# Kernel optimization log

Measured on AMD Instinct MI355X. Metric: run time of the kernel, lower is better.

The kernel has to match this reference:

```python
import jax, jax.numpy as jnp
import numpy as np

B, C, H, W = 2, 128, 96, 96
HEADS, WIN, M = 4, 7, 16
HD = C // HEADS
N = H * W
K = WIN * WIN


def _unfold(xp, h, w, win):
    wins = jnp.stack([xp[:, :, i:i + h, j:j + w]
                      for i in range(win) for j in range(win)], axis=-1)  # [B,C_,h,w,K]
    b, c = xp.shape[0], xp.shape[1]
    return wins.reshape(b, c, h * w, win * win).transpose(0, 2, 3, 1)


def setup_inputs() -> dict:
    key = jax.random.key(0)
    ks = jax.random.split(key, 12)
    s = 0.02
    return {
        "x": jax.random.normal(ks[0], (B, C, H, W), dtype=jnp.float32),
        "phi": jax.random.normal(ks[1], (B, M, H, W), dtype=jnp.float32),
        "Wq": jax.random.normal(ks[2], (C, C), dtype=jnp.float32) * s,
        "bq": jax.random.normal(ks[3], (C,), dtype=jnp.float32) * s,
        "Wk": jax.random.normal(ks[4], (C, C), dtype=jnp.float32) * s,
        "bk": jax.random.normal(ks[5], (C,), dtype=jnp.float32) * s,
        "Wv": jax.random.normal(ks[6], (C, C), dtype=jnp.float32) * s,
        "bv": jax.random.normal(ks[7], (C,), dtype=jnp.float32) * s,
        "Wo": jax.random.normal(ks[8], (C, C), dtype=jnp.float32) * s,
        "bo": jax.random.normal(ks[9], (C,), dtype=jnp.float32) * s,
        "log_alpha": jnp.zeros((), dtype=jnp.float32),  # alpha = 1.0
        "beta": jnp.full((HEADS,), 0.5, dtype=jnp.float32),
    }


def reference(x, phi, Wq, bq, Wk, bk, Wv, bv, Wo, bo, log_alpha, beta):
    pad = WIN // 2
    scale = HD ** -0.5
    normalizer = np.sqrt(2.0 * M).astype(np.float32)

    x_pad = jnp.pad(x, ((0, 0), (0, 0), (pad, pad), (pad, pad)))
    phi_pad = jnp.pad(phi, ((0, 0), (0, 0), (pad, pad), (pad, pad)), constant_values=1.0)

    x_flat = x.reshape(B, C, N).transpose(0, 2, 1)          # [B,N,C]
    q = (x_flat @ Wq + bq).reshape(B, N, HEADS, HD)

    xu = _unfold(x_pad, H, W, WIN)                          # [B,N,K,C]
    k = (xu @ Wk + bk).reshape(B, N, K, HEADS, HD)
    v = (xu @ Wv + bv).reshape(B, N, K, HEADS, HD)

    logits = jnp.einsum('bnhd,bnkhd->bhnk', q, k) * scale   # [B,HEADS,N,K]

    phi_u = _unfold(phi_pad, H, W, WIN)                     # [B,N,K,M]
    phi_c = phi.reshape(B, M, N).transpose(0, 2, 1)[:, :, None, :]  # [B,N,1,M]
    diff_sq = ((phi_c - phi_u) ** 2).sum(-1)                # [B,N,K]
    log_k_geo = -jnp.exp(log_alpha) * diff_sq / normalizer
    logits = logits + beta[None, :, None, None] * log_k_geo[:, None]

    attn = jax.nn.softmax(logits, axis=-1)                  # [B,HEADS,N,K]
    out = jnp.einsum('bhnk,bnkhd->bnhd', attn, v).reshape(B, N, C)
    out = (out @ Wo + bo).transpose(0, 2, 1).reshape(B, C, H, W)
    return out
```

## Files before the change

kernel.cpp:

```cpp
#include <hip/hip_runtime.h>

typedef unsigned int uint;
typedef __attribute__((ext_vector_type(8))) short bf16x8;
typedef __attribute__((ext_vector_type(4))) float f32x4;

#define B_ 2
#define C_ 128
#define H_ 96
#define W_ 96
#define HEADS_ 4
#define HD_ 32
#define M_ 16
#define WIN_ 7
#define PAD_ 3
#define N_ (H_*W_)
#define HP_ (H_+2*PAD_)
#define HP2_ (HP_*HP_)
#define KW_ (WIN_*WIN_)
#define TILE_ 8
#define HALO_ (TILE_+WIN_-1)
#define NHALO_ (HALO_*HALO_)

static __device__ __forceinline__ uint f2bf(float f) {
    uint u = __float_as_uint(f);
    u = (u + 0x7fffu + ((u >> 16) & 1u)) >> 16;
    return u & 0xffffu;
}
static __device__ __forceinline__ uint pack2(float a, float b) {
    return f2bf(a) | (f2bf(b) << 16);
}
static __device__ __forceinline__ float bf_lo(uint u){ return __uint_as_float(u << 16); }
static __device__ __forceinline__ float bf_hi(uint u){ return __uint_as_float(u & 0xffff0000u); }

static __device__ __forceinline__ float dot2bf(uint a, uint b, float c) {
    float d;
    asm("v_dot2_f32_bf16 %0, %1, %2, %3" : "=v"(d) : "v"(a), "v"(b), "v"(c));
    return d;
}

template<int CTRL>
static __device__ __forceinline__ float dpp_mov(float v) {
    return __int_as_float(__builtin_amdgcn_update_dpp(
        0, __float_as_int(v), CTRL, 0xF, 0xF, false));
}
#define DPP_XOR1(v)  dpp_mov<0xB1>(v)
#define DPP_XOR2(v)  dpp_mov<0x4E>(v)
#define DPP_BCAST0(v) dpp_mov<0x00>(v)
#define DPP_BCAST1(v) dpp_mov<0x55>(v)
#define DPP_BCAST2(v) dpp_mov<0xAA>(v)
#define DPP_BCAST3(v) dpp_mov<0xFF>(v)

#define SWZ(row, c2) ((c2) ^ (((row) & 7) << 2))


__global__ __launch_bounds__(256) void pad_fill(
    const float* __restrict__ phi, const float* __restrict__ bk, const float* __restrict__ bv,
    uint* __restrict__ KVp, float* __restrict__ PhiT)
{
    int idx = blockIdx.x * 256 + threadIdx.x;
    if (idx >= B_*HP2_) return;
    int b  = idx / HP2_;
    int pp = idx % HP2_;
    int py = pp / HP_, px = pp % HP_;
    bool interior = (py >= PAD_ && py < H_+PAD_ && px >= PAD_ && px < W_+PAD_);
    if (!interior) {
        #pragma unroll
        for (int h = 0; h < HEADS_; ++h) {
            size_t base = ((size_t)(b*HEADS_+h)*HP2_ + pp) * 32;
            #pragma unroll
            for (int q4i = 0; q4i < 4; ++q4i) {
                const float* kb8 = bk + h*HD_ + q4i*8;
                const float* vb8 = bv + h*HD_ + q4i*8;
                uint4 ku, vu;
                ku.x = pack2(kb8[0],kb8[1]); ku.y = pack2(kb8[2],kb8[3]);
                ku.z = pack2(kb8[4],kb8[5]); ku.w = pack2(kb8[6],kb8[7]);
                vu.x = pack2(vb8[0],vb8[1]); vu.y = pack2(vb8[2],vb8[3]);
                vu.z = pack2(vb8[4],vb8[5]); vu.w = pack2(vb8[6],vb8[7]);
                ((uint4*)(KVp + base))[q4i]     = ku;
                ((uint4*)(KVp + base))[4 + q4i] = vu;
            }
        }
    }
    size_t pb = ((size_t)b*HP2_ + pp) * M_;
    if (interior) {
        int y = py - PAD_, xx = px - PAD_;
        #pragma unroll
        for (int m = 0; m < M_; ++m)
            PhiT[pb + m] = phi[((size_t)b*M_ + m)*N_ + y*W_ + xx];
    } else {
        #pragma unroll
        for (int m = 0; m < M_; ++m) PhiT[pb + m] = 1.0f;
    }
}

__global__ __launch_bounds__(256, 3) void qkv_proj(
    const float* __restrict__ x,
    const float* __restrict__ Wq, const float* __restrict__ bq,
    const float* __restrict__ Wk, const float* __restrict__ bk,
    const float* __restrict__ Wv, const float* __restrict__ bv,
    float* __restrict__ Qp, uint* __restrict__ KVp)
{
    __shared__ uint ldsA[128*64];
    __shared__ uint ldsB[64*64];

    const int t  = threadIdx.x;
    const int n0 = blockIdx.x * 64;
    const int b  = blockIdx.y;
    const int pj = blockIdx.z;
    const float* Wsrc = (pj == 0) ? Wq : (pj == 1) ? Wk : Wv;
    const float* bsrc = (pj == 0) ? bq : (pj == 1) ? bk : bv;

    for (int idx = t; idx < 128*64; idx += 256) {
        int co = idx & 127, c2 = idx >> 7;
        float w0 = Wsrc[(size_t)(2*c2  )*C_ + co];
        float w1 = Wsrc[(size_t)(2*c2+1)*C_ + co];
        ldsA[co*64 + SWZ(co, c2)] = pack2(w0, w1);
    }
    const float* xb = x + (size_t)b*C_*N_;
    for (int idx = t; idx < 64*64; idx += 256) {
        int pix = idx & 63, c2 = idx >> 6;
        float a0 = xb[(size_t)(2*c2  )*N_ + n0 + pix];
        float a1 = xb[(size_t)(2*c2+1)*N_ + n0 + pix];
        ldsB[pix*64 + SWZ(pix, c2)] = pack2(a0, a1);
    }
    __syncthreads();

    const int lane = t & 63, w = t >> 6;
    const int q = lane >> 4, r16 = lane & 15;
    const int sw = (r16 & 7) << 2;

    f32x4 acc[2][4];
    #pragma unroll
    for (int cf = 0; cf < 2; ++cf) {
        float4 b4 = *(const float4*)(bsrc + (2*w+cf)*16 + q*4);
        f32x4 bi = {b4.x, b4.y, b4.z, b4.w};
        #pragma unroll
        for (int pf = 0; pf < 4; ++pf) acc[cf][pf] = bi;
    }

    #pragma unroll
    for (int kk = 0; kk < 4; ++kk) {
        int kbase = kk*16 + q*4;
        bf16x8 af[2], bfr[4];
        #pragma unroll
        for (int cf = 0; cf < 2; ++cf) {
            int row = (2*w+cf)*16 + r16;
            af[cf] = *(const bf16x8*)&ldsA[row*64 + (kbase ^ sw)];
        }
        #pragma unroll
        for (int pf = 0; pf < 4; ++pf) {
            int row = pf*16 + r16;
            bfr[pf] = *(const bf16x8*)&ldsB[row*64 + (kbase ^ sw)];
        }
        #pragma unroll
        for (int cf = 0; cf < 2; ++cf)
            #pragma unroll
            for (int pf = 0; pf < 4; ++pf)
                acc[cf][pf] = __builtin_amdgcn_mfma_f32_16x16x32_bf16(
                    af[cf], bfr[pf], acc[cf][pf], 0, 0, 0);
    }

    if (pj == 0) {
        #pragma unroll
        for (int pf = 0; pf < 4; ++pf) {
            int n = n0 + pf*16 + r16;
            #pragma unroll
            for (int cf = 0; cf < 2; ++cf) {
                int co0 = (2*w+cf)*16 + q*4;
                *(f32x4*)(Qp + ((size_t)b*N_ + n)*C_ + co0) = acc[cf][pf];
            }
        }
    } else {
        int rowb[4];
        #pragma unroll
        for (int pf = 0; pf < 4; ++pf) {
            int n = n0 + pf*16 + r16;
            int y = n / W_, xx = n - y*W_;
            rowb[pf] = (y+PAD_)*HP_ + xx + PAD_;
        }
        const int ubase = (pj == 1) ? 0 : 16;
        #pragma unroll
        for (int cf = 0; cf < 2; ++cf) {
            int co0 = (2*w+cf)*16 + q*4;
            int h   = co0 >> 5;
            int u   = ubase + ((co0 & 31) >> 1);
            uint* kvb = KVp + (size_t)(b*HEADS_+h)*HP2_*32;
            #pragma unroll
            for (int pf = 0; pf < 4; ++pf) {
                uint2 uu;
                uu.x = pack2(acc[cf][pf][0], acc[cf][pf][1]);
                uu.y = pack2(acc[cf][pf][2], acc[cf][pf][3]);
                *(uint2*)(kvb + (size_t)rowb[pf]*32 + u) = uu;
            }
        }
    }
}

__global__ __launch_bounds__(256, 3) void attn(
    const float* __restrict__ Qp, const uint* __restrict__ KVp,
    const float* __restrict__ PhiT, const float* __restrict__ log_alpha,
    const float* __restrict__ beta, float* __restrict__ AO)
{
    __shared__ uint4  kl[NHALO_*4];
    __shared__ uint4  vl[NHALO_*4];
    __shared__ float4 pl[NHALO_*4];

    const int t  = threadIdx.x;
    const int h  = blockIdx.y;
    const int b  = blockIdx.z;
    const int bx = blockIdx.x;
    const int tile = ((bx & 7) * 18) + (bx >> 3);
    const int y0 = (tile / (W_/TILE_)) * TILE_;
    const int x0 = (tile % (W_/TILE_)) * TILE_;

    const uint* kvb = KVp + (size_t)(b*HEADS_+h)*HP2_*32;
    for (int idx = t; idx < NHALO_*8; idx += 256) {
        int hp = idx >> 3, u4 = idx & 7;
        int hy = hp / HALO_, hx = hp % HALO_;
        size_t rowb = (size_t)(y0+hy)*HP_ + (x0+hx);
        uint4 val = *(const uint4*)(kvb + rowb*32 + u4*4);
        if (u4 < 4) kl[hp*4 + u4] = val;
        else        vl[hp*4 + (u4-4)] = val;
    }
    const float* pbase = PhiT + (size_t)b*HP2_*M_;
    for (int idx = t; idx < NHALO_*4; idx += 256) {
        int hp = idx >> 2, sb = idx & 3;
        int hy = hp / HALO_, hx = hp % HALO_;
        size_t rowb = (size_t)(y0+hy)*HP_ + (x0+hx);
        pl[idx] = *(const float4*)(pbase + rowb*M_ + sb*4);
    }
    __syncthreads();

    const int s  = t & 3;
    const int p  = t >> 2;
    const int qy = p >> 3, qx = p & 7;
    const int n  = (y0+qy)*W_ + (x0+qx);
    const bool c1 = (s & 1) != 0;
    const bool c2 = (s & 2) != 0;

    uint qh0, qh1, qh2, qh3, ql0, ql1, ql2, ql3;
    {
        const float* qptr = Qp + ((size_t)b*N_ + n)*C_ + h*HD_ + s*8;
        float4 q0 = ((const float4*)qptr)[0];
        float4 q1 = ((const float4*)qptr)[1];
        float qf[8] = {q0.x, q0.y, q0.z, q0.w, q1.x, q1.y, q1.z, q1.w};
        float rf[8];
        #pragma unroll
        for (int i = 0; i < 8; ++i)
            rf[i] = qf[i] - __uint_as_float(f2bf(qf[i]) << 16);
        qh0 = pack2(qf[0], qf[1]); qh1 = pack2(qf[2], qf[3]);
        qh2 = pack2(qf[4], qf[5]); qh3 = pack2(qf[6], qf[7]);
        ql0 = pack2(rf[0], rf[1]); ql1 = pack2(rf[2], rf[3]);
        ql2 = pack2(rf[4], rf[5]); ql3 = pack2(rf[6], rf[7]);
    }
    float4 pc = pl[((qy+PAD_)*HALO_ + (qx+PAD_))*4 + s];

    const float alpha = __expf(log_alpha[0]);
    const float scale = 0.17677669529663687f;
    const float gcoef = -beta[h] * alpha * 0.17677669529663687f;

    auto partial = [&](int hp) -> float {
        uint4 kw = kl[(hp<<2) + s];
        float da = dot2bf(qh0, kw.x, 0.0f);
        float db = dot2bf(ql0, kw.x, 0.0f);
        da = dot2bf(qh1, kw.y, da);
        db = dot2bf(ql1, kw.y, db);
        da = dot2bf(qh2, kw.z, da);
        db = dot2bf(ql2, kw.z, db);
        da = dot2bf(qh3, kw.w, da);
        db = dot2bf(ql3, kw.w, db);
        float pdot = da + db;
        float4 pv = pl[(hp<<2) + s];
        float d0 = pc.x - pv.x, d1 = pc.y - pv.y;
        float d2 = pc.z - pv.z, d3 = pc.w - pv.w;
        float pdsq = fmaf(d0,d0, fmaf(d1,d1, fmaf(d2,d2, d3*d3)));
        return fmaf(pdot, scale, gcoef*pdsq);
    };

    float lp[13];
    float mx = -1e30f;

#define HPOS(KK) ((qy + (KK)/WIN_)*HALO_ + qx + ((KK)%WIN_))
#define LGROUP(G) { \
    float pr0 = partial(HPOS(4*(G)  )); \
    float pr1 = partial(HPOS(4*(G)+1)); \
    float pr2 = partial(HPOS(4*(G)+2)); \
    float pr3 = partial(HPOS(4*(G)+3)); \
    float Av = (c1 ? pr1 : pr0) + DPP_XOR1(c1 ? pr0 : pr1); \
    float Bv = (c1 ? pr3 : pr2) + DPP_XOR1(c1 ? pr2 : pr3); \
    float lg = (c2 ? Bv : Av) + DPP_XOR2(c2 ? Av : Bv); \
    lp[(G)] = lg; mx = fmaxf(mx, lg); }

    LGROUP(0) LGROUP(1) LGROUP(2) LGROUP(3) LGROUP(4) LGROUP(5)
    LGROUP(6) LGROUP(7) LGROUP(8) LGROUP(9) LGROUP(10) LGROUP(11)
    {
        float pr = partial(HPOS(48));
        pr += DPP_XOR1(pr);
        pr += DPP_XOR2(pr);
        lp[12] = pr; mx = fmaxf(mx, pr);
    }
    mx = fmaxf(mx, DPP_XOR1(mx));
    mx = fmaxf(mx, DPP_XOR2(mx));

    float ssum = 0.f;
#define EXPG(G) { float e = __expf(lp[(G)] - mx); lp[(G)] = e; ssum += e; }
    EXPG(0) EXPG(1) EXPG(2) EXPG(3) EXPG(4) EXPG(5)
    EXPG(6) EXPG(7) EXPG(8) EXPG(9) EXPG(10) EXPG(11)
    {
        float e = (s == 0) ? __expf(lp[12] - mx) : 0.f;
        lp[12] = e; ssum += e;
    }
    ssum += DPP_XOR1(ssum);
    ssum += DPP_XOR2(ssum);
    float inv = 1.0f / ssum;

    float4 o0 = make_float4(0.f,0.f,0.f,0.f);
    float4 o1 = make_float4(0.f,0.f,0.f,0.f);
#define PVPOS(KK, BC) { \
    float wgt = DPP_BCAST##BC(lp[(KK)>>2]); \
    uint4 vw = vl[(HPOS(KK)<<2) + s]; \
    o0.x = fmaf(wgt, bf_lo(vw.x), o0.x); \
    o0.y = fmaf(wgt, bf_hi(vw.x), o0.y); \
    o0.z = fmaf(wgt, bf_lo(vw.y), o0.z); \
    o0.w = fmaf(wgt, bf_hi(vw.y), o0.w); \
    o1.x = fmaf(wgt, bf_lo(vw.z), o1.x); \
    o1.y = fmaf(wgt, bf_hi(vw.z), o1.y); \
    o1.z = fmaf(wgt, bf_lo(vw.w), o1.z); \
    o1.w = fmaf(wgt, bf_hi(vw.w), o1.w); }

    PVPOS(0,0)  PVPOS(1,1)  PVPOS(2,2)  PVPOS(3,3)  PVPOS(4,0)  PVPOS(5,1)  PVPOS(6,2)
    PVPOS(7,3)  PVPOS(8,0)  PVPOS(9,1)  PVPOS(10,2) PVPOS(11,3) PVPOS(12,0) PVPOS(13,1)
    PVPOS(14,2) PVPOS(15,3) PVPOS(16,0) PVPOS(17,1) PVPOS(18,2) PVPOS(19,3) PVPOS(20,0)
    PVPOS(21,1) PVPOS(22,2) PVPOS(23,3) PVPOS(24,0) PVPOS(25,1) PVPOS(26,2) PVPOS(27,3)
    PVPOS(28,0) PVPOS(29,1) PVPOS(30,2) PVPOS(31,3) PVPOS(32,0) PVPOS(33,1) PVPOS(34,2)
    PVPOS(35,3) PVPOS(36,0) PVPOS(37,1) PVPOS(38,2) PVPOS(39,3) PVPOS(40,0) PVPOS(41,1)
    PVPOS(42,2) PVPOS(43,3) PVPOS(44,0) PVPOS(45,1) PVPOS(46,2) PVPOS(47,3) PVPOS(48,0)

    float* aop = AO + ((size_t)b*N_ + n)*C_ + h*HD_ + s*8;
    o0.x *= inv; o0.y *= inv; o0.z *= inv; o0.w *= inv;
    o1.x *= inv; o1.y *= inv; o1.z *= inv; o1.w *= inv;
    ((float4*)aop)[0] = o0;
    ((float4*)aop)[1] = o1;
}

__global__ __launch_bounds__(256, 3) void out_proj(
    const float* __restrict__ AO, const float* __restrict__ Wo,
    const float* __restrict__ bo, float* __restrict__ out)
{
    __shared__ uint ldsA[128*64];
    __shared__ uint ldsB[64*64];

    const int t  = threadIdx.x;
    const int b  = blockIdx.x / (N_/64);
    const int n0 = (blockIdx.x % (N_/64)) * 64;

    for (int idx = t; idx < 128*64; idx += 256) {
        int co = idx & 127, c2 = idx >> 7;
        float w0 = Wo[(size_t)(2*c2  )*C_ + co];
        float w1 = Wo[(size_t)(2*c2+1)*C_ + co];
        ldsA[co*64 + SWZ(co, c2)] = pack2(w0, w1);
    }
    for (int idx = t; idx < 64*32; idx += 256) {
        int pix = idx >> 5, c4 = idx & 31;
        float4 v = ((const float4*)(AO + ((size_t)b*N_ + n0 + pix)*C_))[c4];
        ldsB[pix*64 + SWZ(pix, 2*c4  )] = pack2(v.x, v.y);
        ldsB[pix*64 + SWZ(pix, 2*c4+1)] = pack2(v.z, v.w);
    }
    __syncthreads();

    const int lane = t & 63, w = t >> 6;
    const int q = lane >> 4, r16 = lane & 15;
    const int sw = (r16 & 7) << 2;

    f32x4 acc[2][4];
    #pragma unroll
    for (int cf = 0; cf < 2; ++cf) {
        float4 b4 = *(const float4*)(bo + (2*w+cf)*16 + q*4);
        f32x4 bi = {b4.x, b4.y, b4.z, b4.w};
        #pragma unroll
        for (int pf = 0; pf < 4; ++pf) acc[cf][pf] = bi;
    }

    #pragma unroll
    for (int kk = 0; kk < 4; ++kk) {
        int kbase = kk*16 + q*4;
        bf16x8 af[2], bfr[4];
        #pragma unroll
        for (int cf = 0; cf < 2; ++cf) {
            int row = (2*w+cf)*16 + r16;
            af[cf] = *(const bf16x8*)&ldsA[row*64 + (kbase ^ sw)];
        }
        #pragma unroll
        for (int pf = 0; pf < 4; ++pf) {
            int row = pf*16 + r16;
            bfr[pf] = *(const bf16x8*)&ldsB[row*64 + (kbase ^ sw)];
        }
        #pragma unroll
        for (int cf = 0; cf < 2; ++cf)
            #pragma unroll
            for (int pf = 0; pf < 4; ++pf)
                acc[cf][pf] = __builtin_amdgcn_mfma_f32_16x16x32_bf16(
                    af[cf], bfr[pf], acc[cf][pf], 0, 0, 0);
    }

    #pragma unroll
    for (int cf = 0; cf < 2; ++cf) {
        #pragma unroll
        for (int rr = 0; rr < 4; ++rr) {
            int co = (2*w+cf)*16 + q*4 + rr;
            float* orow = out + ((size_t)b*C_ + co)*N_ + n0;
            #pragma unroll
            for (int pf = 0; pf < 4; ++pf)
                orow[pf*16 + r16] = acc[cf][pf][rr];
        }
    }
}

extern "C" void kernel_launch(void* const* d_in, const int* in_sizes, int n_in,
                              void* d_out, int out_size, void* d_ws, size_t ws_size,
                              hipStream_t stream)
{
    const float* x    = (const float*)d_in[0];
    const float* phi  = (const float*)d_in[1];
    const float* Wq   = (const float*)d_in[2];
    const float* bq   = (const float*)d_in[3];
    const float* Wk   = (const float*)d_in[4];
    const float* bk   = (const float*)d_in[5];
    const float* Wv   = (const float*)d_in[6];
    const float* bv   = (const float*)d_in[7];
    const float* Wo   = (const float*)d_in[8];
    const float* bo   = (const float*)d_in[9];
    const float* la   = (const float*)d_in[10];
    const float* beta = (const float*)d_in[11];
    float* out = (float*)d_out;

    float* ws   = (float*)d_ws;
    float* Qp   = ws;
    uint*  KVp  = (uint*)(Qp + (size_t)B_*N_*C_);
    float* PhiT = (float*)(KVp + (size_t)B_*HEADS_*HP2_*32);
    float* AO   = Qp;

    pad_fill<<<dim3((B_*HP2_ + 255)/256), dim3(256), 0, stream>>>(phi, bk, bv, KVp, PhiT);
    qkv_proj<<<dim3(N_/64, B_, 3), dim3(256), 0, stream>>>(x, Wq, bq, Wk, bk, Wv, bv, Qp, KVp);
    attn<<<dim3((H_/TILE_)*(W_/TILE_), HEADS_, B_), dim3(256), 0, stream>>>(Qp, KVp, PhiT, la, beta, AO);
    out_proj<<<dim3(B_*(N_/64)), dim3(256), 0, stream>>>(AO, Wo, bo, out);
}
```

Measured before the change: 65.96 us.

## Recast local window attention as dense halo MFMA with masking

The attention kernel's per-thread dot2/DPP scalar path is replaced by MFMA bf16 matrix multiplies. Each pixel row is scored against the full 14x14 halo (224 keys) and positions outside its 7x7 window are masked. The geometric term is folded into the matmul by expanding the squared distance (key phi packed into the K tile, -2*gcoef*phi_center into the B operand, key norms precomputed), and P@V becomes a second MFMA over a transposed V tile. This trades about four times more raw FLOPs and larger LDS and register use (56 logits per lane) for matrix-core throughput, and the bf16 split of phi and the cancellation in the expanded distance may lose some accuracy.

```diff
diff --git a/kernel.cpp b/kernel.cpp
--- a/kernel.cpp
+++ b/kernel.cpp
@@ -16,10 +16,7 @@
 #define N_ (H_*W_)
 #define HP_ (H_+2*PAD_)
 #define HP2_ (HP_*HP_)
-#define KW_ (WIN_*WIN_)
 #define TILE_ 8
-#define HALO_ (TILE_+WIN_-1)
-#define NHALO_ (HALO_*HALO_)
 
 static __device__ __forceinline__ uint f2bf(float f) {
     uint u = __float_as_uint(f);
@@ -29,28 +26,10 @@
 static __device__ __forceinline__ uint pack2(float a, float b) {
     return f2bf(a) | (f2bf(b) << 16);
 }
-static __device__ __forceinline__ float bf_lo(uint u){ return __uint_as_float(u << 16); }
-static __device__ __forceinline__ float bf_hi(uint u){ return __uint_as_float(u & 0xffff0000u); }
-
-static __device__ __forceinline__ float dot2bf(uint a, uint b, float c) {
-    float d;
-    asm("v_dot2_f32_bf16 %0, %1, %2, %3" : "=v"(d) : "v"(a), "v"(b), "v"(c));
-    return d;
-}
-
-template<int CTRL>
-static __device__ __forceinline__ float dpp_mov(float v) {
-    return __int_as_float(__builtin_amdgcn_update_dpp(
-        0, __float_as_int(v), CTRL, 0xF, 0xF, false));
-}
-#define DPP_XOR1(v)  dpp_mov<0xB1>(v)
-#define DPP_XOR2(v)  dpp_mov<0x4E>(v)
-#define DPP_BCAST0(v) dpp_mov<0x00>(v)
-#define DPP_BCAST1(v) dpp_mov<0x55>(v)
-#define DPP_BCAST2(v) dpp_mov<0xAA>(v)
-#define DPP_BCAST3(v) dpp_mov<0xFF>(v)
 
 #define SWZ(row, c2) ((c2) ^ (((row) & 7) << 2))
+
+union U4 { uint u[4]; uint4 u4; bf16x8 v; };
 
 
 __global__ __launch_bounds__(256) void pad_fill(
@@ -201,9 +180,9 @@
     const float* __restrict__ PhiT, const float* __restrict__ log_alpha,
     const float* __restrict__ beta, float* __restrict__ AO)
 {
-    __shared__ uint4  kl[NHALO_*4];
-    __shared__ uint4  vl[NHALO_*4];
-    __shared__ float4 pl[NHALO_*4];
+    __shared__ uint  lds0[64*128];
+    __shared__ uint  vtl[32*128];
+    __shared__ float pv2l[224];
 
     const int t  = threadIdx.x;
     const int h  = blockIdx.y;
@@ -213,134 +192,159 @@
     const int y0 = (tile / (W_/TILE_)) * TILE_;
     const int x0 = (tile % (W_/TILE_)) * TILE_;
 
-    const uint* kvb = KVp + (size_t)(b*HEADS_+h)*HP2_*32;
-    for (int idx = t; idx < NHALO_*8; idx += 256) {
-        int hp = idx >> 3, u4 = idx & 7;
-        int hy = hp / HALO_, hx = hp % HALO_;
-        size_t rowb = (size_t)(y0+hy)*HP_ + (x0+hx);
-        uint4 val = *(const uint4*)(kvb + rowb*32 + u4*4);
-        if (u4 < 4) kl[hp*4 + u4] = val;
-        else        vl[hp*4 + (u4-4)] = val;
-    }
-    const float* pbase = PhiT + (size_t)b*HP2_*M_;
-    for (int idx = t; idx < NHALO_*4; idx += 256) {
-        int hp = idx >> 2, sb = idx & 3;
-        int hy = hp / HALO_, hx = hp % HALO_;
-        size_t rowb = (size_t)(y0+hy)*HP_ + (x0+hx);
-        pl[idx] = *(const float4*)(pbase + rowb*M_ + sb*4);
-    }
-    __syncthreads();
-
-    const int s  = t & 3;
-    const int p  = t >> 2;
-    const int qy = p >> 3, qx = p & 7;
-    const int n  = (y0+qy)*W_ + (x0+qx);
-    const bool c1 = (s & 1) != 0;
-    const bool c2 = (s & 2) != 0;
-
-    uint qh0, qh1, qh2, qh3, ql0, ql1, ql2, ql3;
-    {
-        const float* qptr = Qp + ((size_t)b*N_ + n)*C_ + h*HD_ + s*8;
-        float4 q0 = ((const float4*)qptr)[0];
-        float4 q1 = ((const float4*)qptr)[1];
-        float qf[8] = {q0.x, q0.y, q0.z, q0.w, q1.x, q1.y, q1.z, q1.w};
-        float rf[8];
-        #pragma unroll
-        for (int i = 0; i < 8; ++i)
-            rf[i] = qf[i] - __uint_as_float(f2bf(qf[i]) << 16);
-        qh0 = pack2(qf[0], qf[1]); qh1 = pack2(qf[2], qf[3]);
-        qh2 = pack2(qf[4], qf[5]); qh3 = pack2(qf[6], qf[7]);
-        ql0 = pack2(rf[0], rf[1]); ql1 = pack2(rf[2], rf[3]);
-        ql2 = pack2(rf[4], rf[5]); ql3 = pack2(rf[6], rf[7]);
-    }
-    float4 pc = pl[((qy+PAD_)*HALO_ + (qx+PAD_))*4 + s];
-
     const float alpha = __expf(log_alpha[0]);
     const float scale = 0.17677669529663687f;
     const float gcoef = -beta[h] * alpha * 0.17677669529663687f;
 
-    auto partial = [&](int hp) -> float {
-        uint4 kw = kl[(hp<<2) + s];
-        float da = dot2bf(qh0, kw.x, 0.0f);
-        float db = dot2bf(ql0, kw.x, 0.0f);
-        da = dot2bf(qh1, kw.y, da);
-        db = dot2bf(ql1, kw.y, db);
-        da = dot2bf(qh2, kw.z, da);
-        db = dot2bf(ql2, kw.z, db);
-        da = dot2bf(qh3, kw.w, da);
-        db = dot2bf(ql3, kw.w, db);
-        float pdot = da + db;
-        float4 pv = pl[(hp<<2) + s];
-        float d0 = pc.x - pv.x, d1 = pc.y - pv.y;
-        float d2 = pc.z - pv.z, d3 = pc.w - pv.w;
-        float pdsq = fmaf(d0,d0, fmaf(d1,d1, fmaf(d2,d2, d3*d3)));
-        return fmaf(pdot, scale, gcoef*pdsq);
-    };
-
-    float lp[13];
+    const uint*  kvb = KVp + (size_t)(b*HEADS_+h)*HP2_*32;
+    const float* phb = PhiT + (size_t)b*HP2_*M_;
+
+    for (int idx = t; idx < 224*32; idx += 256) {
+        int row = idx >> 5, colu = idx & 31;
+        int ky = row >> 4, kx = row & 15;
+        uint val = 0;
+        if (kx < 14) {
+            size_t rowb = (size_t)(y0+ky)*HP_ + (x0+kx);
+            if (colu < 16) {
+                val = kvb[rowb*32 + colu];
+            } else if (colu < 24) {
+                const float* pp = phb + rowb*M_ + (colu-16)*2;
+                val = pack2(pp[0], pp[1]);
+            }
+        }
+        lds0[row*32 + SWZ(row, colu)] = val;
+    }
+    for (int idx = t; idx < 16*128; idx += 256) {
+        int kv2 = idx & 127, p = idx >> 7;
+        if (kv2 >= 112) continue;
+        uint a = 0, c = 0;
+        if ((kv2 & 7) != 7) {
+            int kv0 = kv2*2;
+            int ky = kv0 >> 4, kx = kv0 & 15;
+            size_t rowb = (size_t)(y0+ky)*HP_ + (x0+kx);
+            a = kvb[rowb*32 + 16 + p];
+            c = kvb[rowb*32 + 48 + p];
+        }
+        int ch0 = p*2;
+        uint lo = (a & 0xffffu) | (c << 16);
+        uint hi = (a >> 16) | (c & 0xffff0000u);
+        vtl[ch0*128     + SWZ(ch0,   kv2)] = lo;
+        vtl[(ch0+1)*128 + SWZ(ch0+1, kv2)] = hi;
+    }
+    for (int idx = t; idx < 224; idx += 256) {
+        int ky = idx >> 4, kx = idx & 15;
+        float s = 0.f;
+        if (kx < 14) {
+            const float* pp = phb + ((size_t)(y0+ky)*HP_ + (x0+kx))*M_;
+            #pragma unroll
+            for (int m4 = 0; m4 < 4; ++m4) {
+                float4 v = ((const float4*)pp)[m4];
+                s = fmaf(v.x,v.x, fmaf(v.y,v.y, fmaf(v.z,v.z, fmaf(v.w,v.w, s))));
+            }
+            s *= gcoef;
+        }
+        pv2l[idx] = s;
+    }
+
+    const int lane = t & 63, w = t >> 6;
+    const int qq = lane >> 4, r16 = lane & 15;
+    const int pix = w*16 + r16, py = pix >> 3, px = pix & 7;
+    const int n = (y0+py)*W_ + (x0+px);
+
+    U4 Bh0, Bl0, Bh1, Bl1;
+    {
+        const float* qp = Qp + ((size_t)b*N_ + n)*C_ + h*HD_ + qq*8;
+        float4 qa = ((const float4*)qp)[0];
+        float4 qb = ((const float4*)qp)[1];
+        float v[8] = {qa.x*scale, qa.y*scale, qa.z*scale, qa.w*scale,
+                      qb.x*scale, qb.y*scale, qb.z*scale, qb.w*scale};
+        #pragma unroll
+        for (int i = 0; i < 4; ++i) {
+            float a0 = v[2*i], a1 = v[2*i+1];
+            float r0 = a0 - __uint_as_float(f2bf(a0) << 16);
+            float r1 = a1 - __uint_as_float(f2bf(a1) << 16);
+            Bh0.u[i] = pack2(a0, a1);
+            Bl0.u[i] = pack2(r0, r1);
+            Bh1.u[i] = 0u; Bl1.u[i] = 0u;
+        }
+        if (qq < 2) {
+            const float* pcp = phb + ((size_t)(y0+py+PAD_)*HP_ + (x0+px+PAD_))*M_ + qq*8;
+            const float m2g = -2.0f * gcoef;
+            #pragma unroll
+            for (int i = 0; i < 4; ++i) {
+                float a0 = pcp[2*i]*m2g, a1 = pcp[2*i+1]*m2g;
+                float r0 = a0 - __uint_as_float(f2bf(a0) << 16);
+                float r1 = a1 - __uint_as_float(f2bf(a1) << 16);
+                Bh1.u[i] = pack2(a0, a1);
+                Bl1.u[i] = pack2(r0, r1);
+            }
+        }
+    }
+    __syncthreads();
+
+    const int sw = (r16 & 7) << 2;
+    const int c0 = (qq*4) ^ sw;
+    const int c1 = (16 + qq*4) ^ sw;
+
+    float lp[56];
     float mx = -1e30f;
-
-#define HPOS(KK) ((qy + (KK)/WIN_)*HALO_ + qx + ((KK)%WIN_))
-#define LGROUP(G) { \
-    float pr0 = partial(HPOS(4*(G)  )); \
-    float pr1 = partial(HPOS(4*(G)+1)); \
-    float pr2 = partial(HPOS(4*(G)+2)); \
-    float pr3 = partial(HPOS(4*(G)+3)); \
-    float Av = (c1 ? pr1 : pr0) + DPP_XOR1(c1 ? pr0 : pr1); \
-    float Bv = (c1 ? pr3 : pr2) + DPP_XOR1(c1 ? pr2 : pr3); \
-    float lg = (c2 ? Bv : Av) + DPP_XOR2(c2 ? Av : Bv); \
-    lp[(G)] = lg; mx = fmaxf(mx, lg); }
-
-    LGROUP(0) LGROUP(1) LGROUP(2) LGROUP(3) LGROUP(4) LGROUP(5)
-    LGROUP(6) LGROUP(7) LGROUP(8) LGROUP(9) LGROUP(10) LGROUP(11)
-    {
-        float pr = partial(HPOS(48));
-        pr += DPP_XOR1(pr);
-        pr += DPP_XOR2(pr);
-        lp[12] = pr; mx = fmaxf(mx, pr);
-    }
-    mx = fmaxf(mx, DPP_XOR1(mx));
-    mx = fmaxf(mx, DPP_XOR2(mx));
-
+    #pragma unroll
+    for (int f = 0; f < 14; ++f) {
+        const uint* arow = lds0 + (f*16 + r16)*32;
+        bf16x8 A0 = *(const bf16x8*)(arow + c0);
+        bf16x8 A1 = *(const bf16x8*)(arow + c1);
+        f32x4 ah = {0.f,0.f,0.f,0.f}, al = {0.f,0.f,0.f,0.f};
+        ah = __builtin_amdgcn_mfma_f32_16x16x32_bf16(A0, Bh0.v, ah, 0,0,0);
+        ah = __builtin_amdgcn_mfma_f32_16x16x32_bf16(A1, Bh1.v, ah, 0,0,0);
+        al = __builtin_amdgcn_mfma_f32_16x16x32_bf16(A0, Bl0.v, al, 0,0,0);
+        al = __builtin_amdgcn_mfma_f32_16x16x32_bf16(A1, Bl1.v, al, 0,0,0);
+        #pragma unroll
+        for (int r = 0; r < 4; ++r) {
+            int kx = qq*4 + r;
+            float lg = ah[r] + al[r] + pv2l[f*16 + kx];
+            bool ok = ((uint)(f - py) < 7u) && ((uint)(kx - px) < 7u);
+            lg = ok ? lg : -1e30f;
+            lp[f*4+r] = lg;
+            mx = fmaxf(mx, lg);
+        }
+    }
+    mx = fmaxf(mx, __shfl_xor(mx, 16));
+    mx = fmaxf(mx, __shfl_xor(mx, 32));
     float ssum = 0.f;
-#define EXPG(G) { float e = __expf(lp[(G)] - mx); lp[(G)] = e; ssum += e; }
-    EXPG(0) EXPG(1) EXPG(2) EXPG(3) EXPG(4) EXPG(5)
-    EXPG(6) EXPG(7) EXPG(8) EXPG(9) EXPG(10) EXPG(11)
-    {
-        float e = (s == 0) ? __expf(lp[12] - mx) : 0.f;
-        lp[12] = e; ssum += e;
-    }
-    ssum += DPP_XOR1(ssum);
-    ssum += DPP_XOR2(ssum);
+    #pragma unroll
+    for (int i = 0; i < 56; ++i) { float e = __expf(lp[i]-mx); lp[i] = e; ssum += e; }
+    ssum += __shfl_xor(ssum, 16);
+    ssum += __shfl_xor(ssum, 32);
     float inv = 1.0f / ssum;
 
-    float4 o0 = make_float4(0.f,0.f,0.f,0.f);
-    float4 o1 = make_float4(0.f,0.f,0.f,0.f);
-#define PVPOS(KK, BC) { \
-    float wgt = DPP_BCAST##BC(lp[(KK)>>2]); \
-    uint4 vw = vl[(HPOS(KK)<<2) + s]; \
-    o0.x = fmaf(wgt, bf_lo(vw.x), o0.x); \
-    o0.y = fmaf(wgt, bf_hi(vw.x), o0.y); \
-    o0.z = fmaf(wgt, bf_lo(vw.y), o0.z); \
-    o0.w = fmaf(wgt, bf_hi(vw.y), o0.w); \
-    o1.x = fmaf(wgt, bf_lo(vw.z), o1.x); \
-    o1.y = fmaf(wgt, bf_hi(vw.z), o1.y); \
-    o1.z = fmaf(wgt, bf_lo(vw.w), o1.z); \
-    o1.w = fmaf(wgt, bf_hi(vw.w), o1.w); }
-
-    PVPOS(0,0)  PVPOS(1,1)  PVPOS(2,2)  PVPOS(3,3)  PVPOS(4,0)  PVPOS(5,1)  PVPOS(6,2)
-    PVPOS(7,3)  PVPOS(8,0)  PVPOS(9,1)  PVPOS(10,2) PVPOS(11,3) PVPOS(12,0) PVPOS(13,1)
-    PVPOS(14,2) PVPOS(15,3) PVPOS(16,0) PVPOS(17,1) PVPOS(18,2) PVPOS(19,3) PVPOS(20,0)
-    PVPOS(21,1) PVPOS(22,2) PVPOS(23,3) PVPOS(24,0) PVPOS(25,1) PVPOS(26,2) PVPOS(27,3)
-    PVPOS(28,0) PVPOS(29,1) PVPOS(30,2) PVPOS(31,3) PVPOS(32,0) PVPOS(33,1) PVPOS(34,2)
-    PVPOS(35,3) PVPOS(36,0) PVPOS(37,1) PVPOS(38,2) PVPOS(39,3) PVPOS(40,0) PVPOS(41,1)
-    PVPOS(42,2) PVPOS(43,3) PVPOS(44,0) PVPOS(45,1) PVPOS(46,2) PVPOS(47,3) PVPOS(48,0)
-
-    float* aop = AO + ((size_t)b*N_ + n)*C_ + h*HD_ + s*8;
-    o0.x *= inv; o0.y *= inv; o0.z *= inv; o0.w *= inv;
-    o1.x *= inv; o1.y *= inv; o1.z *= inv; o1.w *= inv;
-    ((float4*)aop)[0] = o0;
-    ((float4*)aop)[1] = o1;
+    __syncthreads();
+
+    uint* prow = lds0 + (size_t)pix*128;
+    #pragma unroll
+    for (int f = 0; f < 14; ++f) {
+        uint u0 = pack2(lp[f*4+0]*inv, lp[f*4+1]*inv);
+        uint u1 = pack2(lp[f*4+2]*inv, lp[f*4+3]*inv);
+        *(uint2*)(prow + ((f*8 + qq*2) ^ sw)) = make_uint2(u0, u1);
+    }
+
+    #pragma unroll
+    for (int chf = 0; chf < 2; ++chf) {
+        f32x4 acc = {0.f,0.f,0.f,0.f};
+        const uint* vrow = vtl + (chf*16 + r16)*128;
+        #pragma unroll
+        for (int ks = 0; ks < 7; ++ks) {
+            int kb = (ks*16 + qq*4) ^ sw;
+            bf16x8 Af = *(const bf16x8*)(prow + kb);
+            bf16x8 Bf = *(const bf16x8*)(vrow + kb);
+            acc = __builtin_amdgcn_mfma_f32_16x16x32_bf16(Af, Bf, acc, 0,0,0);
+        }
+        #pragma unroll
+        for (int r = 0; r < 4; ++r) {
+            int pixr = w*16 + qq*4 + r;
+            int nr = (y0 + (pixr>>3))*W_ + x0 + (pixr&7);
+            AO[((size_t)b*N_ + nr)*C_ + h*HD_ + chf*16 + r16] = acc[r];
+        }
+    }
 }
 
 __global__ __launch_bounds__(256, 3) void out_proj(
```

After: 89.19 us. 35.2% more time.
